# Kernel tuning notes

Hardware: AMD Instinct MI355X
Metric: run time of the kernel (lower is better)

The kernel has to match this reference:

```python
import jax, jax.numpy as jnp
import numpy as np

VOCAB = 128
D = 256            # word_vec_d
H = 8              # attention heads
DH = D // H
FF = 4 * D
MAX_CHARS = 16
MAX_WORDS = 8
N_NAMES = 2048
N_LAYERS = 2
_n_words = (np.arange(N_NAMES) % MAX_WORDS) + 1   # ragged words-per-name, static
TOTAL_WORDS = int(_n_words.sum())                 # 9216


def _layernorm(x, s, b):
    m = x.mean(-1, keepdims=True)
    v = ((x - m) ** 2).mean(-1, keepdims=True)
    return (x - m) * jax.lax.rsqrt(v + 1e-5) * s + b


def _layer(x, Wqkv, Wo, ln1s, ln1b, W1, W2, ln2s, ln2b, key_pad):
    # x: [B, T, D]; post-LN transformer encoder layer
    B, T, d = x.shape
    q, k, v = jnp.split(x @ Wqkv, 3, axis=-1)
    q = q.reshape(B, T, H, DH).transpose(0, 2, 1, 3)  # [B,H,T,DH]
    k = k.reshape(B, T, H, DH).transpose(0, 2, 1, 3)
    v = v.reshape(B, T, H, DH).transpose(0, 2, 1, 3)
    scores = jnp.einsum('bhtd,bhsd->bhts', q, k) * (1.0 / np.sqrt(DH))
    if key_pad is not None:
        scores = jnp.where(key_pad[:, None, None, :], -1e9, scores)
    p = jax.nn.softmax(scores, axis=-1)
    o = jnp.einsum('bhts,bhsd->bhtd', p, v).transpose(0, 2, 1, 3).reshape(B, T, d)
    x = _layernorm(x + o @ Wo, ln1s, ln1b)
    x = _layernorm(x + jax.nn.gelu(x @ W1) @ W2, ln2s, ln2b)
    return x


def _encode(x, Wqkv, Wo, ln1s, ln1b, W1, W2, ln2s, ln2b, key_pad):
    for l in range(N_LAYERS):  # fixed small layer count
        x = _layer(x, Wqkv[l], Wo[l], ln1s[l], ln1b[l], W1[l], W2[l], ln2s[l], ln2b[l], key_pad)
    return x


def _forward(inputs, word2name, word_pos, char_emb, pos_emb,
             we_Wqkv, we_Wo, we_ln1_s, we_ln1_b, we_W1, we_W2, we_ln2_s, we_ln2_b,
             ne_Wqkv, ne_Wo, ne_ln1_s, ne_ln1_b, ne_W1, ne_W2, ne_ln2_s, ne_ln2_b):
    mask = inputs == 0                                # [W, C] char padding mask
    x = char_emb[inputs] + pos_emb[None]              # [W, C, D]
    word_ft = _encode(x, we_Wqkv, we_Wo, we_ln1_s, we_ln1_b, we_W1, we_W2, we_ln2_s, we_ln2_b, mask)
    not_pad = (~mask)[..., None].astype(word_ft.dtype)
    word_vec = (word_ft * not_pad).sum(1) / not_pad.sum(1)      # masked mean over chars -> [W, D]
    # fused ragged pad/reshape: scatter each word into its (name, slot); pad slots stay zero
    name_emb = jnp.zeros((N_NAMES, MAX_WORDS, D), word_vec.dtype).at[word2name, word_pos].set(word_vec)
    y = _encode(name_emb, ne_Wqkv, ne_Wo, ne_ln1_s, ne_ln1_b, ne_W1, ne_W2, ne_ln2_s, ne_ln2_b, None)
    np2 = (name_emb != 0).astype(y.dtype)             # elementwise pad mask, as in original
    name_ft = (y * np2).sum(1) / np2.sum(1)           # masked mean over word slots -> [N, D]
    return name_ft


def setup_inputs() -> dict:
    rng = np.random.default_rng(0)
    char_len = rng.integers(1, MAX_CHARS + 1, TOTAL_WORDS)      # every word has >=1 char
    chars = rng.integers(1, VOCAB, (TOTAL_WORDS, MAX_CHARS))
    inputs = np.where(np.arange(MAX_CHARS)[None, :] < char_len[:, None], chars, 0).astype(np.int32)
    word2name = np.repeat(np.arange(N_NAMES), _n_words).astype(np.int32)
    word_pos = np.concatenate([np.arange(k) for k in _n_words]).astype(np.int32)

    ks = iter(jax.random.split(jax.random.key(0), 24))
    def nrm(shape):
        return jax.random.normal(next(ks), shape, jnp.float32) * 0.02
    L = N_LAYERS
    return dict(
        inputs=jnp.asarray(inputs), word2name=jnp.asarray(word2name), word_pos=jnp.asarray(word_pos),
        char_emb=nrm((VOCAB, D)), pos_emb=nrm((MAX_CHARS, D)),
        we_Wqkv=nrm((L, D, 3 * D)), we_Wo=nrm((L, D, D)),
        we_ln1_s=jnp.ones((L, D)), we_ln1_b=jnp.zeros((L, D)),
        we_W1=nrm((L, D, FF)), we_W2=nrm((L, FF, D)),
        we_ln2_s=jnp.ones((L, D)), we_ln2_b=jnp.zeros((L, D)),
        ne_Wqkv=nrm((L, D, 3 * D)), ne_Wo=nrm((L, D, D)),
        ne_ln1_s=jnp.ones((L, D)), ne_ln1_b=jnp.zeros((L, D)),
        ne_W1=nrm((L, D, FF)), ne_W2=nrm((L, FF, D)),
        ne_ln2_s=jnp.ones((L, D)), ne_ln2_b=jnp.zeros((L, D)),
    )


def reference(inputs, word2name, word_pos, char_emb, pos_emb,
              we_Wqkv, we_Wo, we_ln1_s, we_ln1_b, we_W1, we_W2, we_ln2_s, we_ln2_b,
              ne_Wqkv, ne_Wo, ne_ln1_s, ne_ln1_b, ne_W1, ne_W2, ne_ln2_s, ne_ln2_b):
    return _forward(inputs, word2name, word_pos, char_emb, pos_emb,
                    we_Wqkv, we_Wo, we_ln1_s, we_ln1_b, we_W1, we_W2, we_ln2_s, we_ln2_b,
                    ne_Wqkv, ne_Wo, ne_ln1_s, ne_ln1_b, ne_W1, ne_W2, ne_ln2_s, ne_ln2_b)
```

## Files before the change

### kernel.cpp

```cpp
#include <hip/hip_runtime.h>
#include <hip/hip_bf16.h>

using short8 = __attribute__((ext_vector_type(8))) short;
using f32x4  = __attribute__((ext_vector_type(4))) float;

#define DEV __device__ __forceinline__
#define LDB 264

DEV float bu(unsigned short u) { union { unsigned int i; float f; } z; z.i = (unsigned)u << 16; return z.f; }
DEV unsigned short fb(float f) { __hip_bfloat16 h = __float2bfloat16(f); return *reinterpret_cast<unsigned short*>(&h); }

DEV float gelu_f(float v) {
    float u = 0.7978845608028654f * (v + 0.044715f * v * v * v);
    u = fminf(fmaxf(u, -20.f), 20.f);
    float e = __expf(2.f * u);
    return 0.5f * v * (1.f + (e - 1.f) / (e + 1.f));
}

__global__ void k_wt(const float* __restrict__ W, unsigned short* __restrict__ WT, int K, int N) {
    int i = blockIdx.x * 256 + threadIdx.x;
    if (i >= N * K) return;
    int n = i / K, k = i % K;
    WT[i] = fb(W[(size_t)k * N + n]);
}

template<int NT, int KG>
DEV void mm64(const unsigned short* __restrict__ A, const unsigned short* __restrict__ B,
              int ldB, int koff, f32x4 acc[NT][4], int nt0, int lane)
{
    const int fl = lane & 15, fh = lane >> 4;
#pragma unroll
    for (int kg = 0; kg < KG; ++kg) {
        short8 b[NT];
#pragma unroll
        for (int i = 0; i < NT; ++i)
            b[i] = *(const short8*)(B + (size_t)((nt0 + i) * 16 + fl) * ldB + koff + kg * 32 + fh * 8);
        short8 a[4];
#pragma unroll
        for (int m = 0; m < 4; ++m)
            a[m] = *(const short8*)(A + (m * 16 + fl) * LDB + kg * 32 + fh * 8);
#pragma unroll
        for (int i = 0; i < NT; ++i)
#pragma unroll
            for (int m = 0; m < 4; ++m)
                acc[i][m] = __builtin_amdgcn_mfma_f32_16x16x32_bf16(a[m], b[i], acc[i][m], 0, 0, 0);
    }
}

template<int NT, bool GEL>
DEV void store_bf16(f32x4 acc[NT][4], unsigned short* __restrict__ D, int nt0, int lane) {
    const int fl = lane & 15, r0 = (lane >> 4) * 4;
#pragma unroll
    for (int i = 0; i < NT; ++i)
#pragma unroll
        for (int m = 0; m < 4; ++m)
#pragma unroll
            for (int r = 0; r < 4; ++r) {
                float v = acc[i][m][r];
                if (GEL) v = gelu_f(v);
                D[(m * 16 + r0 + r) * LDB + (nt0 + i) * 16 + fl] = fb(v);
            }
}

DEV void ln_reg(float xr[4][4][2], const float* __restrict__ s, const float* __restrict__ b,
                unsigned short* __restrict__ xb, float red[64][8],
                float* mrow, float* srow, int tid, int fl, int fh, int wid)
{
    float ps[4][4];
#pragma unroll
    for (int m = 0; m < 4; ++m)
#pragma unroll
        for (int r = 0; r < 4; ++r) {
            float v = xr[m][r][0] + xr[m][r][1];
#pragma unroll
            for (int off = 8; off >= 1; off >>= 1) v += __shfl_xor(v, off, 64);
            ps[m][r] = v;
        }
    if (fl == 0)
#pragma unroll
        for (int m = 0; m < 4; ++m)
#pragma unroll
            for (int r = 0; r < 4; ++r) red[m * 16 + fh * 4 + r][wid] = ps[m][r];
    __syncthreads();
    if (tid < 64) {
        float sum = 0.f;
#pragma unroll
        for (int j = 0; j < 8; ++j) sum += red[tid][j];
        mrow[tid] = sum * (1.f / 256.f);
    }
    __syncthreads();
#pragma unroll
    for (int m = 0; m < 4; ++m)
#pragma unroll
        for (int r = 0; r < 4; ++r) {
            float mu = mrow[m * 16 + fh * 4 + r];
            float d0 = xr[m][r][0] - mu, d1 = xr[m][r][1] - mu;
            float v = d0 * d0 + d1 * d1;
#pragma unroll
            for (int off = 8; off >= 1; off >>= 1) v += __shfl_xor(v, off, 64);
            ps[m][r] = v;
        }
    if (fl == 0)
#pragma unroll
        for (int m = 0; m < 4; ++m)
#pragma unroll
            for (int r = 0; r < 4; ++r) red[m * 16 + fh * 4 + r][wid] = ps[m][r];
    __syncthreads();
    if (tid < 64) {
        float sum = 0.f;
#pragma unroll
        for (int j = 0; j < 8; ++j) sum += red[tid][j];
        srow[tid] = rsqrtf(sum * (1.f / 256.f) + 1e-5f);
    }
    __syncthreads();
    float sc[2], bc[2];
#pragma unroll
    for (int i = 0; i < 2; ++i) { int c = (wid * 2 + i) * 16 + fl; sc[i] = s[c]; bc[i] = b[c]; }
#pragma unroll
    for (int m = 0; m < 4; ++m)
#pragma unroll
        for (int r = 0; r < 4; ++r) {
            int row = m * 16 + fh * 4 + r;
            float mu = mrow[row], rs = srow[row];
#pragma unroll
            for (int i = 0; i < 2; ++i) {
                float v = (xr[m][r][i] - mu) * rs * sc[i] + bc[i];
                xr[m][r][i] = v;
                xb[row * LDB + (wid * 2 + i) * 16 + fl] = fb(v);
            }
        }
    __syncthreads();
}

template<bool WORD>
__global__ __launch_bounds__(512, 1) void k_enc64(
    const int* __restrict__ inputs,
    const float* __restrict__ char_emb, const float* __restrict__ pos_emb,
    const unsigned short* __restrict__ qkvT, const unsigned short* __restrict__ woT,
    const unsigned short* __restrict__ w1T,  const unsigned short* __restrict__ w2T,
    const float* __restrict__ ln1s, const float* __restrict__ ln1b,
    const float* __restrict__ ln2s, const float* __restrict__ ln2b,
    const int* __restrict__ w2n, const int* __restrict__ wpos,
    float* __restrict__ NE, float* __restrict__ out)
{
    constexpr int T = WORD ? 16 : 8;
    const int blk = blockIdx.x, tid = threadIdx.x;
    const int lane = tid & 63, wid = tid >> 6;
    const int fl = lane & 15, fh = lane >> 4;
    __shared__ __attribute__((aligned(16))) unsigned short xb[64 * LDB];
    __shared__ __attribute__((aligned(16))) unsigned short S1[64 * LDB];
    __shared__ __attribute__((aligned(16))) unsigned short S2[64 * LDB];
    __shared__ float red[64][8];
    __shared__ float mrow[64], srow[64];
    __shared__ int ch[64];

    const int wl = WORD ? (tid >> 7) : (tid >> 6);
    const int hh = WORD ? ((tid >> 4) & 7) : ((tid >> 3) & 7);
    const int tt = WORD ? (tid & 15) : (tid & 7);
    const int arow = wl * T + tt;

    float xr[4][4][2];

    if (WORD) {
        if (tid < 64) ch[tid] = inputs[blk * 64 + tid];
        __syncthreads();
#pragma unroll
        for (int m = 0; m < 4; ++m)
#pragma unroll
            for (int r = 0; r < 4; ++r) {
                int row = m * 16 + fh * 4 + r;
#pragma unroll
                for (int i = 0; i < 2; ++i) {
                    int col = (wid * 2 + i) * 16 + fl;
                    float v = char_emb[(size_t)ch[row] * 256 + col] + pos_emb[(row & 15) * 256 + col];
                    xr[m][r][i] = v;
                    xb[row * LDB + col] = fb(v);
                }
            }
    } else {
#pragma unroll
        for (int m = 0; m < 4; ++m)
#pragma unroll
            for (int r = 0; r < 4; ++r) {
                int row = m * 16 + fh * 4 + r;
#pragma unroll
                for (int i = 0; i < 2; ++i) {
                    int col = (wid * 2 + i) * 16 + fl;
                    float v = NE[((size_t)blk * 64 + row) * 256 + col];
                    xr[m][r][i] = v;
                    xb[row * LDB + col] = fb(v);
                }
            }
    }
    __syncthreads();

    for (int l = 0; l < 2; ++l) {
        const unsigned short* wq = qkvT + (size_t)l * 196608;
        const unsigned short* wk = wq + 65536;
        const unsigned short* wv = wq + 131072;
        const unsigned short* wo = woT + (size_t)l * 65536;
        const unsigned short* w1 = w1T + (size_t)l * 262144;
        const unsigned short* w2 = w2T + (size_t)l * 262144;

        { f32x4 acc[2][4] = {}; mm64<2, 8>(xb, wq, 256, 0, acc, wid * 2, lane); store_bf16<2, false>(acc, S1, wid * 2, lane); }
        { f32x4 acc[2][4] = {}; mm64<2, 8>(xb, wk, 256, 0, acc, wid * 2, lane); store_bf16<2, false>(acc, S2, wid * 2, lane); }
        __syncthreads();

        float q[32], p[T];
        {
#pragma unroll
            for (int db = 0; db < 4; ++db) {
                short8 qv = *(const short8*)&S1[arow * LDB + hh * 32 + db * 8];
#pragma unroll
                for (int j = 0; j < 8; ++j) q[db * 8 + j] = bu((unsigned short)qv[j]);
            }
            float mx = -1e30f;
#pragma unroll
            for (int s = 0; s < T; ++s) {
                float dot = 0.f;
#pragma unroll
                for (int db = 0; db < 4; ++db) {
                    short8 kv = *(const short8*)&S2[(wl * T + s) * LDB + hh * 32 + db * 8];
#pragma unroll
                    for (int j = 0; j < 8; ++j) dot += q[db * 8 + j] * bu((unsigned short)kv[j]);
                }
                dot *= 0.17677669529663687f;
                if (WORD && ch[wl * 16 + s] == 0) dot = -1e9f;
                p[s] = dot; mx = fmaxf(mx, dot);
            }
            float sum = 0.f;
#pragma unroll
            for (int s = 0; s < T; ++s) { p[s] = __expf(p[s] - mx); sum += p[s]; }
            float inv = 1.f / sum;
#pragma unroll
            for (int s = 0; s < T; ++s) p[s] *= inv;
        }
        __syncthreads();

        { f32x4 acc[2][4] = {}; mm64<2, 8>(xb, wv, 256, 0, acc, wid * 2, lane); store_bf16<2, false>(acc, S1, wid * 2, lane); }
        __syncthreads();

        {
            float o[32];
#pragma unroll
            for (int j = 0; j < 32; ++j) o[j] = 0.f;
#pragma unroll
            for (int s = 0; s < T; ++s) {
                float ps = p[s];
#pragma unroll
                for (int db = 0; db < 4; ++db) {
                    short8 vv = *(const short8*)&S1[(wl * T + s) * LDB + hh * 32 + db * 8];
#pragma unroll
                    for (int j = 0; j < 8; ++j) o[db * 8 + j] += ps * bu((unsigned short)vv[j]);
                }
            }
#pragma unroll
            for (int db = 0; db < 4; ++db) {
                short8 ov;
#pragma unroll
                for (int j = 0; j < 8; ++j) ov[j] = (short)fb(o[db * 8 + j]);
                *(short8*)&S2[arow * LDB + hh * 32 + db * 8] = ov;
            }
        }
        __syncthreads();

        { f32x4 acc[2][4] = {}; mm64<2, 8>(S2, wo, 256, 0, acc, wid * 2, lane);
#pragma unroll
          for (int i = 0; i < 2; ++i)
#pragma unroll
              for (int m = 0; m < 4; ++m)
#pragma unroll
                  for (int r = 0; r < 4; ++r) xr[m][r][i] += acc[i][m][r]; }
        __syncthreads();
        ln_reg(xr, ln1s + l * 256, ln1b + l * 256, xb, red, mrow, srow, tid, fl, fh, wid);

        {
            f32x4 acc2[2][4] = {};
            for (int c = 0; c < 4; ++c) {
                f32x4 acc1[2][4] = {};
                mm64<2, 8>(xb, w1 + (size_t)c * 65536, 256, 0, acc1, wid * 2, lane);
                store_bf16<2, true>(acc1, S1, wid * 2, lane);
                __syncthreads();
                mm64<2, 8>(S1, w2, 1024, c * 256, acc2, wid * 2, lane);
                __syncthreads();
            }
#pragma unroll
            for (int i = 0; i < 2; ++i)
#pragma unroll
                for (int m = 0; m < 4; ++m)
#pragma unroll
                    for (int r = 0; r < 4; ++r) xr[m][r][i] += acc2[i][m][r];
        }
        ln_reg(xr, ln2s + l * 256, ln2b + l * 256, xb, red, mrow, srow, tid, fl, fh, wid);
    }

    if (WORD) {
#pragma unroll
        for (int m = 0; m < 4; ++m) {
            int cnt = 0;
#pragma unroll
            for (int c = 0; c < 16; ++c) if (ch[m * 16 + c] != 0) ++cnt;
            float inv = 1.f / (float)cnt;
#pragma unroll
            for (int i = 0; i < 2; ++i) {
                float s = 0.f;
#pragma unroll
                for (int r = 0; r < 4; ++r)
                    if (ch[m * 16 + fh * 4 + r] != 0) s += xr[m][r][i];
                s += __shfl_xor(s, 16, 64);
                s += __shfl_xor(s, 32, 64);
                if (fh == 0) {
                    int wg = blk * 4 + m;
                    size_t nrow = (size_t)w2n[wg] * 8 + wpos[wg];
                    NE[nrow * 256 + (wid * 2 + i) * 16 + fl] = s * inv;
                }
            }
        }
    } else {
#pragma unroll
        for (int m = 0; m < 4; ++m)
#pragma unroll
            for (int i = 0; i < 2; ++i) {
                int col = (wid * 2 + i) * 16 + fl;
                float s = 0.f, c = 0.f;
#pragma unroll
                for (int r = 0; r < 4; ++r) {
                    int row = m * 16 + fh * 4 + r;
                    float nev = NE[((size_t)blk * 64 + row) * 256 + col];
                    if (nev != 0.f) { s += xr[m][r][i]; c += 1.f; }
                }
                s += __shfl_xor(s, 16, 64);
                c += __shfl_xor(c, 16, 64);
                if ((fh & 1) == 0) {
                    int name = blk * 8 + 2 * m + (fh >> 1);
                    out[(size_t)name * 256 + col] = (c > 0.f) ? s / c : 0.f;
                }
            }
    }
}

extern "C" void kernel_launch(void* const* d_in, const int* in_sizes, int n_in,
                              void* d_out, int out_size, void* d_ws, size_t ws_size,
                              hipStream_t stream) {
    float* out = (float*)d_out;

    const int* inputs    = (const int*)d_in[0];
    const int* w2n       = (const int*)d_in[1];
    const int* wpos      = (const int*)d_in[2];
    const float* char_emb = (const float*)d_in[3];
    const float* pos_emb  = (const float*)d_in[4];
    const float* we_Wqkv = (const float*)d_in[5];
    const float* we_Wo   = (const float*)d_in[6];
    const float* we_ln1s = (const float*)d_in[7];
    const float* we_ln1b = (const float*)d_in[8];
    const float* we_W1   = (const float*)d_in[9];
    const float* we_W2   = (const float*)d_in[10];
    const float* we_ln2s = (const float*)d_in[11];
    const float* we_ln2b = (const float*)d_in[12];
    const float* ne_Wqkv = (const float*)d_in[13];
    const float* ne_Wo   = (const float*)d_in[14];
    const float* ne_ln1s = (const float*)d_in[15];
    const float* ne_ln1b = (const float*)d_in[16];
    const float* ne_W1   = (const float*)d_in[17];
    const float* ne_W2   = (const float*)d_in[18];
    const float* ne_ln2s = (const float*)d_in[19];
    const float* ne_ln2b = (const float*)d_in[20];

    char* ws = (char*)d_ws;
    size_t off = 0;
    auto alloc = [&](size_t bytes) { void* p = ws + off; off += (bytes + 255) & ~(size_t)255; return p; };
    float* NE = (float*)alloc((size_t)16384 * 256 * 4);
    unsigned short* qkvT_we = (unsigned short*)alloc((size_t)2 * 196608 * 2);
    unsigned short* woT_we  = (unsigned short*)alloc((size_t)2 * 65536 * 2);
    unsigned short* w1T_we  = (unsigned short*)alloc((size_t)2 * 262144 * 2);
    unsigned short* w2T_we  = (unsigned short*)alloc((size_t)2 * 262144 * 2);
    unsigned short* qkvT_ne = (unsigned short*)alloc((size_t)2 * 196608 * 2);
    unsigned short* woT_ne  = (unsigned short*)alloc((size_t)2 * 65536 * 2);
    unsigned short* w1T_ne  = (unsigned short*)alloc((size_t)2 * 262144 * 2);
    unsigned short* w2T_ne  = (unsigned short*)alloc((size_t)2 * 262144 * 2);

    for (int l = 0; l < 2; ++l) {
        k_wt<<<(196608 + 255) / 256, 256, 0, stream>>>(we_Wqkv + (size_t)l * 196608, qkvT_we + (size_t)l * 196608, 256, 768);
        k_wt<<<(65536  + 255) / 256, 256, 0, stream>>>(we_Wo   + (size_t)l * 65536,  woT_we  + (size_t)l * 65536,  256, 256);
        k_wt<<<(262144 + 255) / 256, 256, 0, stream>>>(we_W1   + (size_t)l * 262144, w1T_we  + (size_t)l * 262144, 256, 1024);
        k_wt<<<(262144 + 255) / 256, 256, 0, stream>>>(we_W2   + (size_t)l * 262144, w2T_we  + (size_t)l * 262144, 1024, 256);
        k_wt<<<(196608 + 255) / 256, 256, 0, stream>>>(ne_Wqkv + (size_t)l * 196608, qkvT_ne + (size_t)l * 196608, 256, 768);
        k_wt<<<(65536  + 255) / 256, 256, 0, stream>>>(ne_Wo   + (size_t)l * 65536,  woT_ne  + (size_t)l * 65536,  256, 256);
        k_wt<<<(262144 + 255) / 256, 256, 0, stream>>>(ne_W1   + (size_t)l * 262144, w1T_ne  + (size_t)l * 262144, 256, 1024);
        k_wt<<<(262144 + 255) / 256, 256, 0, stream>>>(ne_W2   + (size_t)l * 262144, w2T_ne  + (size_t)l * 262144, 1024, 256);
    }

    (void)hipMemsetAsync(NE, 0, (size_t)16384 * 256 * 4, stream);

    k_enc64<true><<<2304, 512, 0, stream>>>(inputs, char_emb, pos_emb,
                                            qkvT_we, woT_we, w1T_we, w2T_we,
                                            we_ln1s, we_ln1b, we_ln2s, we_ln2b,
                                            w2n, wpos, NE, nullptr);

    k_enc64<false><<<256, 512, 0, stream>>>(nullptr, nullptr, nullptr,
                                            qkvT_ne, woT_ne, w1T_ne, w2T_ne,
                                            ne_ln1s, ne_ln1b, ne_ln2s, ne_ln2b,
                                            nullptr, nullptr, NE, out);
}
```

Measured before the change: 1.553 ms.

## Fuse QKV projection, merge attention phases, and widen FFN chunks to cut barriers

Computes Q, K and V projections in one pass that shares A-fragment loads, stores V into the xb buffer so score and PV computation run in one phase, and processes the FFN in two 512-wide chunks using both scratch buffers instead of four 256-wide chunks. This halves the FFN barrier count and removes several syncs in attention. The launch bound now requests two blocks per CU, which may force register spilling given the larger accumulator arrays (24 for QKV, 16+8 for FFN).

Measured after the change: 1.686 ms. 1.09x slower.

```diff
diff --git a/kernel.cpp b/kernel.cpp
--- a/kernel.cpp
+++ b/kernel.cpp
@@ -47,6 +47,37 @@
     }
 }
 
+DEV void mm64_qkv(const unsigned short* __restrict__ A,
+                  const unsigned short* __restrict__ wq, const unsigned short* __restrict__ wk,
+                  const unsigned short* __restrict__ wv,
+                  f32x4 aq[2][4], f32x4 ak[2][4], f32x4 av[2][4], int nt0, int lane)
+{
+    const int fl = lane & 15, fh = lane >> 4;
+#pragma unroll
+    for (int kg = 0; kg < 8; ++kg) {
+        short8 a[4];
+#pragma unroll
+        for (int m = 0; m < 4; ++m)
+            a[m] = *(const short8*)(A + (m * 16 + fl) * LDB + kg * 32 + fh * 8);
+        short8 bq[2], bk[2], bv[2];
+#pragma unroll
+        for (int i = 0; i < 2; ++i) {
+            size_t rowoff = (size_t)((nt0 + i) * 16 + fl) * 256 + kg * 32 + fh * 8;
+            bq[i] = *(const short8*)(wq + rowoff);
+            bk[i] = *(const short8*)(wk + rowoff);
+            bv[i] = *(const short8*)(wv + rowoff);
+        }
+#pragma unroll
+        for (int i = 0; i < 2; ++i)
+#pragma unroll
+            for (int m = 0; m < 4; ++m) {
+                aq[i][m] = __builtin_amdgcn_mfma_f32_16x16x32_bf16(a[m], bq[i], aq[i][m], 0, 0, 0);
+                ak[i][m] = __builtin_amdgcn_mfma_f32_16x16x32_bf16(a[m], bk[i], ak[i][m], 0, 0, 0);
+                av[i][m] = __builtin_amdgcn_mfma_f32_16x16x32_bf16(a[m], bv[i], av[i][m], 0, 0, 0);
+            }
+    }
+}
+
 template<int NT, bool GEL>
 DEV void store_bf16(f32x4 acc[NT][4], unsigned short* __restrict__ D, int nt0, int lane) {
     const int fl = lane & 15, r0 = (lane >> 4) * 4;
@@ -133,7 +164,7 @@
 }
 
 template<bool WORD>
-__global__ __launch_bounds__(512, 1) void k_enc64(
+__global__ __launch_bounds__(512, 2) void k_enc64(
     const int* __restrict__ inputs,
     const float* __restrict__ char_emb, const float* __restrict__ pos_emb,
     const unsigned short* __restrict__ qkvT, const unsigned short* __restrict__ woT,
@@ -202,12 +233,18 @@
         const unsigned short* w1 = w1T + (size_t)l * 262144;
         const unsigned short* w2 = w2T + (size_t)l * 262144;
 
-        { f32x4 acc[2][4] = {}; mm64<2, 8>(xb, wq, 256, 0, acc, wid * 2, lane); store_bf16<2, false>(acc, S1, wid * 2, lane); }
-        { f32x4 acc[2][4] = {}; mm64<2, 8>(xb, wk, 256, 0, acc, wid * 2, lane); store_bf16<2, false>(acc, S2, wid * 2, lane); }
-        __syncthreads();
-
-        float q[32], p[T];
         {
+            f32x4 aq[2][4] = {}, ak[2][4] = {}, av[2][4] = {};
+            mm64_qkv(xb, wq, wk, wv, aq, ak, av, wid * 2, lane);
+            store_bf16<2, false>(aq, S1, wid * 2, lane);
+            store_bf16<2, false>(ak, S2, wid * 2, lane);
+            __syncthreads();
+            store_bf16<2, false>(av, xb, wid * 2, lane);
+            __syncthreads();
+        }
+
+        {
+            float q[32], p[T];
 #pragma unroll
             for (int db = 0; db < 4; ++db) {
                 short8 qv = *(const short8*)&S1[arow * LDB + hh * 32 + db * 8];
@@ -234,13 +271,7 @@
             float inv = 1.f / sum;
 #pragma unroll
             for (int s = 0; s < T; ++s) p[s] *= inv;
-        }
-        __syncthreads();
-
-        { f32x4 acc[2][4] = {}; mm64<2, 8>(xb, wv, 256, 0, acc, wid * 2, lane); store_bf16<2, false>(acc, S1, wid * 2, lane); }
-        __syncthreads();
-
-        {
+
             float o[32];
 #pragma unroll
             for (int j = 0; j < 32; ++j) o[j] = 0.f;
@@ -249,7 +280,7 @@
                 float ps = p[s];
 #pragma unroll
                 for (int db = 0; db < 4; ++db) {
-                    short8 vv = *(const short8*)&S1[(wl * T + s) * LDB + hh * 32 + db * 8];
+                    short8 vv = *(const short8*)&xb[(wl * T + s) * LDB + hh * 32 + db * 8];
 #pragma unroll
                     for (int j = 0; j < 8; ++j) o[db * 8 + j] += ps * bu((unsigned short)vv[j]);
                 }
@@ -259,12 +290,12 @@
                 short8 ov;
 #pragma unroll
                 for (int j = 0; j < 8; ++j) ov[j] = (short)fb(o[db * 8 + j]);
-                *(short8*)&S2[arow * LDB + hh * 32 + db * 8] = ov;
+                *(short8*)&S1[arow * LDB + hh * 32 + db * 8] = ov;
             }
         }
         __syncthreads();
 
-        { f32x4 acc[2][4] = {}; mm64<2, 8>(S2, wo, 256, 0, acc, wid * 2, lane);
+        { f32x4 acc[2][4] = {}; mm64<2, 8>(S1, wo, 256, 0, acc, wid * 2, lane);
 #pragma unroll
           for (int i = 0; i < 2; ++i)
 #pragma unroll
@@ -276,12 +307,25 @@
 
         {
             f32x4 acc2[2][4] = {};
-            for (int c = 0; c < 4; ++c) {
-                f32x4 acc1[2][4] = {};
-                mm64<2, 8>(xb, w1 + (size_t)c * 65536, 256, 0, acc1, wid * 2, lane);
-                store_bf16<2, true>(acc1, S1, wid * 2, lane);
+#pragma unroll
+            for (int sc = 0; sc < 2; ++sc) {
+                f32x4 a1[4][4] = {};
+                mm64<4, 8>(xb, w1, 256, 0, a1, sc * 32 + wid * 4, lane);
+                const int r0 = fh * 4;
+#pragma unroll
+                for (int i = 0; i < 4; ++i) {
+                    int tl = wid * 4 + i;
+                    unsigned short* buf = (tl < 16) ? S1 : S2;
+                    int col0 = (tl & 15) * 16 + fl;
+#pragma unroll
+                    for (int m = 0; m < 4; ++m)
+#pragma unroll
+                        for (int r = 0; r < 4; ++r)
+                            buf[(m * 16 + r0 + r) * LDB + col0] = fb(gelu_f(a1[i][m][r]));
+                }
                 __syncthreads();
-                mm64<2, 8>(S1, w2, 1024, c * 256, acc2, wid * 2, lane);
+                mm64<2, 8>(S1, w2, 1024, sc * 512,       acc2, wid * 2, lane);
+                mm64<2, 8>(S2, w2, 1024, sc * 512 + 256, acc2, wid * 2, lane);
                 __syncthreads();
             }
 #pragma unroll
```
